# Kernel optimization log

Hardware: AMD Instinct MI355X
Metric: run time of the kernel (lower is better)

The kernel has to match this reference:

```python
import jax, jax.numpy as jnp
import numpy as np
import math

B, N, D, O, H = 8, 1024, 512, 512, 8
HD = O // H  # head_dim = 64


def setup_inputs() -> dict:
    key = jax.random.key(0)
    ks = jax.random.split(key, 12)
    x = jax.random.normal(ks[0], (B, N, D), dtype=jnp.float32)
    adj = jax.random.uniform(ks[1], (B, N, N), dtype=jnp.float32)  # unused by forward math
    mask = jax.random.randint(ks[2], (B, N), 0, 2) > 0  # bool padding mask
    # learned params (torch nn.Linear: y = x @ W.T + b)
    qkv_w = jax.random.normal(ks[3], (3 * O, D), dtype=jnp.float32) / math.sqrt(D)
    qkv_b = jnp.zeros((3 * O,), dtype=jnp.float32)
    # self_loop_W: 1/head_dim + U(0,1), per head, non-trainable
    self_loop_W = (1.0 / HD + jax.random.uniform(ks[4], (1, H, 1, 1))).astype(jnp.float32)
    w1 = jax.random.normal(ks[5], (O, O), dtype=jnp.float32) / math.sqrt(O)
    b1 = jnp.zeros((O,), dtype=jnp.float32)
    w2 = jax.random.normal(ks[6], (O, O), dtype=jnp.float32) / math.sqrt(O)
    b2 = jnp.zeros((O,), dtype=jnp.float32)
    wr = jax.random.normal(ks[7], (O, D), dtype=jnp.float32) / math.sqrt(D)
    br = jnp.zeros((O,), dtype=jnp.float32)
    return {"x": x, "adj": adj, "mask": mask, "self_loop_W": self_loop_W,
            "qkv_w": qkv_w, "qkv_b": qkv_b, "w1": w1, "b1": b1,
            "w2": w2, "b2": b2, "wr": wr, "br": br}


def reference(x, adj, mask, self_loop_W, qkv_w, qkv_b, w1, b1, w2, b2, wr, br):
    fmask = mask.astype(x.dtype)  # [B,N]
    # --- MoireAttention ---
    qkv = x @ qkv_w.T + qkv_b                       # [B,N,3O]
    qkv = qkv.reshape(B, N, 3, H, HD).transpose(2, 0, 3, 1, 4)  # [3,B,H,N,hd]
    Q, K, V = qkv[0], qkv[1], qkv[2]
    scores = jnp.einsum('bhnd,bhmd->bhnm', Q, K) / math.sqrt(HD)  # [B,H,N,N]
    eye = jnp.eye(N, dtype=scores.dtype)
    scores = scores + eye[None, None] * self_loop_W  # per-head diagonal self-loop bias
    mask2d = mask[:, None, :, None] & mask[:, None, None, :]  # [B,1,N,N]
    scores = jnp.where(mask2d, scores, jnp.asarray(-1e6, scores.dtype))
    attn = jax.nn.softmax(scores, axis=-1)
    h = jnp.einsum('bhnm,bhmd->bhnd', attn, V)      # [B,H,N,hd]
    h = h.transpose(0, 2, 1, 3).reshape(B, N, O)
    # --- mask, FFN (eval mode: noise/dropout are identity), mask ---
    h = h * fmask[..., None]
    h = jax.nn.relu(h @ w1.T + b1) @ w2.T + b2
    h = h * fmask[..., None]
    # --- residual blend ---
    x_proj = x @ wr.T + br
    return h * 0.5 + x_proj * 0.5
```

## Files before the change

### kernel.cpp

```cpp
#include <hip/hip_runtime.h>
#include <hip/hip_bf16.h>

typedef __attribute__((ext_vector_type(8))) short short8;
typedef __attribute__((ext_vector_type(4))) float f32x4;
typedef __attribute__((ext_vector_type(4))) short short4v;

#define BB 8
#define NN 1024
#define DD 512
#define OO 512
#define HH 8
#define HD 64
#define MM (BB * NN)

#define SEG_N 10
struct ConvArgs {
  const float* src[SEG_N];
  __hip_bfloat16* dst[SEG_N];
  int n4[SEG_N];
};

__global__ void convert_kernel(ConvArgs a) {
  const int t = blockIdx.y;
  const int n4 = a.n4[t];
  const float4* fs = (const float4*)a.src[t];
  short4v* d = (short4v*)a.dst[t];
  for (int i = blockIdx.x * blockDim.x + threadIdx.x; i < n4;
       i += gridDim.x * blockDim.x) {
    const float4 v = fs[i];
    union { short4v s; __hip_bfloat16 h[4]; } u;
    u.h[0] = __float2bfloat16(v.x);
    u.h[1] = __float2bfloat16(v.y);
    u.h[2] = __float2bfloat16(v.z);
    u.h[3] = __float2bfloat16(v.w);
    d[i] = u.s;
  }
}

template <int MODE>
__global__ __launch_bounds__(256) void gemm_bt(
    const __hip_bfloat16* __restrict__ A0, const __hip_bfloat16* __restrict__ B0,
    const __hip_bfloat16* __restrict__ A1, const __hip_bfloat16* __restrict__ B1,
    const __hip_bfloat16* __restrict__ bias0, const __hip_bfloat16* __restrict__ bias1,
    const int* __restrict__ mask,
    __hip_bfloat16* __restrict__ out0, __hip_bfloat16* __restrict__ out1,
    __hip_bfloat16* __restrict__ out2, float* __restrict__ outf,
    int M, int N, int Kd) {
  __shared__ __hip_bfloat16 As[128 * 40];
  __shared__ __hip_bfloat16 Bs[128 * 40];

  const int tid  = threadIdx.x;
  const int wave = tid >> 6;
  const int lane = tid & 63;
  const int fl   = lane & 15;
  const int fk   = (lane >> 4) * 8;
  const int wm   = (wave & 1) * 64;
  const int wn   = (wave >> 1) * 64;
  const int m0   = blockIdx.y * 128;
  const int n0   = blockIdx.x * 128;
  const int srow = tid >> 2;
  const int scol = (tid & 3) * 8;

  f32x4 acc[4][4];
#pragma unroll
  for (int i = 0; i < 4; ++i)
#pragma unroll
    for (int j = 0; j < 4; ++j) acc[i][j] = (f32x4){0.f, 0.f, 0.f, 0.f};

  const int npairs = (MODE == 2) ? 2 : 1;
  for (int p = 0; p < npairs; ++p) {
    const __hip_bfloat16* Ap = (p == 0) ? A0 : A1;
    const __hip_bfloat16* Bp = (p == 0) ? B0 : B1;
    for (int k0 = 0; k0 < Kd; k0 += 32) {
      __syncthreads();
      uint4 av0 = *(const uint4*)(Ap + (size_t)(m0 + srow) * Kd + k0 + scol);
      uint4 av1 = *(const uint4*)(Ap + (size_t)(m0 + srow + 64) * Kd + k0 + scol);
      uint4 bv0 = *(const uint4*)(Bp + (size_t)(n0 + srow) * Kd + k0 + scol);
      uint4 bv1 = *(const uint4*)(Bp + (size_t)(n0 + srow + 64) * Kd + k0 + scol);
      *(uint4*)&As[srow * 40 + scol] = av0;
      *(uint4*)&As[(srow + 64) * 40 + scol] = av1;
      *(uint4*)&Bs[srow * 40 + scol] = bv0;
      *(uint4*)&Bs[(srow + 64) * 40 + scol] = bv1;
      __syncthreads();

      short8 af[4], bfr[4];
#pragma unroll
      for (int i = 0; i < 4; ++i)
        af[i] = *(const short8*)&As[(wm + i * 16 + fl) * 40 + fk];
#pragma unroll
      for (int j = 0; j < 4; ++j)
        bfr[j] = *(const short8*)&Bs[(wn + j * 16 + fl) * 40 + fk];
#pragma unroll
      for (int i = 0; i < 4; ++i)
#pragma unroll
        for (int j = 0; j < 4; ++j)
          acc[i][j] = __builtin_amdgcn_mfma_f32_16x16x32_bf16(af[i], bfr[j],
                                                              acc[i][j], 0, 0, 0);
    }
  }

  const int rb = (lane >> 4) * 4;

  if (MODE == 0) {
#pragma unroll
    for (int j = 0; j < 4; ++j) {
      const int colb  = n0 + wn + j * 16;
      const int part  = colb >> 9;
      const int o     = colb & 511;
      const int headq = o >> 6;
      const int d     = (o & 63) + fl;
      const float bi  = __bfloat162float(bias0[colb + fl]);
      if (part < 2) {
        __hip_bfloat16* dst = (part == 0) ? out0 : out1;
#pragma unroll
        for (int i = 0; i < 4; ++i) {
#pragma unroll
          for (int r = 0; r < 4; ++r) {
            const int row = m0 + wm + i * 16 + rb + r;
            const int bb  = row >> 10;
            const int nn  = row & 1023;
            dst[((size_t)((bb << 3) + headq) * NN + nn) * HD + d] =
                __float2bfloat16(acc[i][j][r] + bi);
          }
        }
      } else {
#pragma unroll
        for (int i = 0; i < 4; ++i) {
#pragma unroll
          for (int r = 0; r < 4; ++r) {
            const int row = m0 + wm + i * 16 + rb + r;
            const int bb  = row >> 10;
            const int nn  = row & 1023;
            out2[((size_t)((bb << 3) + headq) * HD + d) * NN + nn] =
                __float2bfloat16(acc[i][j][r] + bi);
          }
        }
      }
    }
  } else if (MODE == 1) {
#pragma unroll
    for (int j = 0; j < 4; ++j) {
      const int col  = n0 + wn + j * 16 + fl;
      const float bi = __bfloat162float(bias0[col]);
#pragma unroll
      for (int i = 0; i < 4; ++i) {
#pragma unroll
        for (int r = 0; r < 4; ++r) {
          const int row = m0 + wm + i * 16 + rb + r;
          float v = fmaxf(acc[i][j][r] + bi, 0.f);
          if (mask[row] == 0) v = 0.f;
          out0[(size_t)row * N + col] = __float2bfloat16(v);
        }
      }
    }
  } else {
#pragma unroll
    for (int j = 0; j < 4; ++j) {
      const int col   = n0 + wn + j * 16 + fl;
      const float b2v = __bfloat162float(bias0[col]);
      const float brv = __bfloat162float(bias1[col]);
#pragma unroll
      for (int i = 0; i < 4; ++i) {
#pragma unroll
        for (int r = 0; r < 4; ++r) {
          const int row = m0 + wm + i * 16 + rb + r;
          const float v = acc[i][j][r] + brv + (mask[row] != 0 ? b2v : 0.f);
          outf[(size_t)row * N + col] = 0.5f * v;
        }
      }
    }
  }
}

__global__ __launch_bounds__(256) void attn_kernel(
    const __hip_bfloat16* __restrict__ Qb, const __hip_bfloat16* __restrict__ Kb,
    const __hip_bfloat16* __restrict__ Vt, const __hip_bfloat16* __restrict__ slw,
    const int* __restrict__ mask, __hip_bfloat16* __restrict__ hb) {
  __shared__ __hip_bfloat16 Qs[64 * 72];
  __shared__ __hip_bfloat16 Ks[64 * 72];
  __shared__ __hip_bfloat16 Vs[64 * 72];
  __shared__ __hip_bfloat16 Ps[64 * 72];
  __shared__ __hip_bfloat16 Ms[NN];

  const int tid  = threadIdx.x;
  const int wave = tid >> 6;
  const int lane = tid & 63;
  const int fl   = lane & 15;
  const int fk   = (lane >> 4) * 8;
  const int rb   = (lane >> 4) * 4;
  const int bh   = blockIdx.x >> 4;
  const int qblk = blockIdx.x & 15;
  const int b    = bh >> 3;
  const int head = bh & 7;
  const int q0   = qblk * 64;

  const float slw_h = __bfloat162float(slw[head]);

  const int srow = tid >> 2;
  const int sc   = (tid & 3) * 8;
  {
    const __hip_bfloat16* qg = Qb + ((size_t)bh * NN + q0) * HD;
    uint4 v0 = *(const uint4*)(qg + srow * HD + sc);
    uint4 v1 = *(const uint4*)(qg + srow * HD + sc + 32);
    *(uint4*)&Qs[srow * 72 + sc] = v0;
    *(uint4*)&Qs[srow * 72 + sc + 32] = v1;
#pragma unroll
    for (int k = 0; k < 4; ++k) {
      const int idx = tid * 4 + k;
      Ms[idx] = __float2bfloat16(mask[b * NN + idx] != 0 ? 1.f : 0.f);
    }
  }
  __syncthreads();
  const short8 qa0 = *(const short8*)&Qs[(wave * 16 + fl) * 72 + fk];
  const short8 qa1 = *(const short8*)&Qs[(wave * 16 + fl) * 72 + fk + 32];

  float lsum[4] = {0.f, 0.f, 0.f, 0.f};
  f32x4 Oacc[4];
#pragma unroll
  for (int t = 0; t < 4; ++t) Oacc[t] = (f32x4){0.f, 0.f, 0.f, 0.f};

  const float L2E = 1.44269504f;
  const float NEG = -11.54156032f;

  for (int kb = 0; kb < NN / 64; ++kb) {
    const int kbase = kb * 64;
    __syncthreads();
    {
      const __hip_bfloat16* kg = Kb + ((size_t)bh * NN + kbase) * HD;
      uint4 v0 = *(const uint4*)(kg + srow * HD + sc);
      uint4 v1 = *(const uint4*)(kg + srow * HD + sc + 32);
      *(uint4*)&Ks[srow * 72 + sc] = v0;
      *(uint4*)&Ks[srow * 72 + sc + 32] = v1;
      const __hip_bfloat16* vg = Vt + ((size_t)bh * HD + srow) * NN + kbase;
      uint4 w0 = *(const uint4*)(vg + sc);
      uint4 w1 = *(const uint4*)(vg + sc + 32);
      *(uint4*)&Vs[srow * 72 + sc] = w0;
      *(uint4*)&Vs[srow * 72 + sc + 32] = w1;
    }
    __syncthreads();

    f32x4 sfr[4];
#pragma unroll
    for (int j = 0; j < 4; ++j) {
      const short8 kf0 = *(const short8*)&Ks[(j * 16 + fl) * 72 + fk];
      const short8 kf1 = *(const short8*)&Ks[(j * 16 + fl) * 72 + fk + 32];
      f32x4 z = (f32x4){0.f, 0.f, 0.f, 0.f};
      z = __builtin_amdgcn_mfma_f32_16x16x32_bf16(qa0, kf0, z, 0, 0, 0);
      z = __builtin_amdgcn_mfma_f32_16x16x32_bf16(qa1, kf1, z, 0, 0, 0);
      sfr[j] = z;
    }

    float mv[4];
#pragma unroll
    for (int j = 0; j < 4; ++j)
      mv[j] = __bfloat162float(Ms[kbase + j * 16 + fl]);

#pragma unroll
    for (int r = 0; r < 4; ++r) {
      const int qrow_l = wave * 16 + rb + r;
      const int qrow_g = q0 + qrow_l;
#pragma unroll
      for (int j = 0; j < 4; ++j) {
        const int col_g = kbase + j * 16 + fl;
        float sv = sfr[j][r] * 0.125f;
        if (col_g == qrow_g) sv += slw_h;
        const float pv = mv[j] * exp2f(fmaf(sv, L2E, NEG));
        lsum[r] += pv;
        Ps[qrow_l * 72 + j * 16 + fl] = __float2bfloat16(pv);
      }
    }

    const short8 pa0 = *(const short8*)&Ps[(wave * 16 + fl) * 72 + fk];
    const short8 pa1 = *(const short8*)&Ps[(wave * 16 + fl) * 72 + fk + 32];
#pragma unroll
    for (int t = 0; t < 4; ++t) {
      const short8 vf0 = *(const short8*)&Vs[(t * 16 + fl) * 72 + fk];
      const short8 vf1 = *(const short8*)&Vs[(t * 16 + fl) * 72 + fk + 32];
      Oacc[t] = __builtin_amdgcn_mfma_f32_16x16x32_bf16(pa0, vf0, Oacc[t], 0, 0, 0);
      Oacc[t] = __builtin_amdgcn_mfma_f32_16x16x32_bf16(pa1, vf1, Oacc[t], 0, 0, 0);
    }
  }

  float scl[4];
#pragma unroll
  for (int r = 0; r < 4; ++r) {
    float l = lsum[r];
#pragma unroll
    for (int off = 1; off < 16; off <<= 1) l += __shfl_xor(l, off, 64);
    const int qrow_g = q0 + wave * 16 + rb + r;
    const float qm = (mask[b * NN + qrow_g] != 0) ? 1.f : 0.f;
    scl[r] = qm / fmaxf(l, 1e-30f);
  }
#pragma unroll
  for (int t = 0; t < 4; ++t) {
    const int d = t * 16 + fl;
#pragma unroll
    for (int r = 0; r < 4; ++r) {
      const int qrow_g = q0 + wave * 16 + rb + r;
      hb[(size_t)(b * NN + qrow_g) * OO + head * HD + d] =
          __float2bfloat16(Oacc[t][r] * scl[r]);
    }
  }
}

extern "C" void kernel_launch(void* const* d_in, const int* in_sizes, int n_in,
                              void* d_out, int out_size, void* d_ws, size_t ws_size,
                              hipStream_t stream) {
  const float* x_raw    = (const float*)d_in[0];
  const int* mask       = (const int*)d_in[2];
  const float* slw_raw  = (const float*)d_in[3];
  const float* qkvw_raw = (const float*)d_in[4];
  const float* qkvb_raw = (const float*)d_in[5];
  const float* w1_raw   = (const float*)d_in[6];
  const float* b1_raw   = (const float*)d_in[7];
  const float* w2_raw   = (const float*)d_in[8];
  const float* b2_raw   = (const float*)d_in[9];
  const float* wr_raw   = (const float*)d_in[10];
  const float* br_raw   = (const float*)d_in[11];
  float* outf           = (float*)d_out;

  __hip_bfloat16* p = (__hip_bfloat16*)d_ws;
  __hip_bfloat16* xc    = p; p += (size_t)MM * DD;
  __hip_bfloat16* qkvwc = p; p += 3 * OO * DD;
  __hip_bfloat16* w1c   = p; p += OO * OO;
  __hip_bfloat16* w2c   = p; p += OO * OO;
  __hip_bfloat16* wrc   = p; p += OO * DD;
  __hip_bfloat16* qkvbc = p; p += 3 * OO;
  __hip_bfloat16* b1c   = p; p += OO;
  __hip_bfloat16* b2c   = p; p += OO;
  __hip_bfloat16* brc   = p; p += OO;
  __hip_bfloat16* slwc  = p; p += 64;
  const size_t ebuf = (size_t)BB * HH * NN * HD;
  __hip_bfloat16* Qb = p; p += ebuf;
  __hip_bfloat16* Kb = p; p += ebuf;
  __hip_bfloat16* Vb = p; p += ebuf;
  __hip_bfloat16* hb = (__hip_bfloat16*)d_out;
  __hip_bfloat16* tb = Kb;

  if (ws_size < (size_t)((char*)p - (char*)d_ws)) return;

  ConvArgs ca;
  ca.src[0] = x_raw;    ca.dst[0] = xc;    ca.n4[0] = MM * DD / 4;
  ca.src[1] = qkvw_raw; ca.dst[1] = qkvwc; ca.n4[1] = 3 * OO * DD / 4;
  ca.src[2] = w1_raw;   ca.dst[2] = w1c;   ca.n4[2] = OO * OO / 4;
  ca.src[3] = w2_raw;   ca.dst[3] = w2c;   ca.n4[3] = OO * OO / 4;
  ca.src[4] = wr_raw;   ca.dst[4] = wrc;   ca.n4[4] = OO * DD / 4;
  ca.src[5] = qkvb_raw; ca.dst[5] = qkvbc; ca.n4[5] = 3 * OO / 4;
  ca.src[6] = b1_raw;   ca.dst[6] = b1c;   ca.n4[6] = OO / 4;
  ca.src[7] = b2_raw;   ca.dst[7] = b2c;   ca.n4[7] = OO / 4;
  ca.src[8] = br_raw;   ca.dst[8] = brc;   ca.n4[8] = OO / 4;
  ca.src[9] = slw_raw;  ca.dst[9] = slwc;  ca.n4[9] = HH / 4;
  convert_kernel<<<dim3(128, SEG_N), 256, 0, stream>>>(ca);

  gemm_bt<0><<<dim3(3 * OO / 128, MM / 128), 256, 0, stream>>>(
      xc, qkvwc, nullptr, nullptr, qkvbc, nullptr, mask, Qb, Kb, Vb, nullptr,
      MM, 3 * OO, DD);
  attn_kernel<<<BB * HH * (NN / 64), 256, 0, stream>>>(Qb, Kb, Vb, slwc, mask, hb);
  gemm_bt<1><<<dim3(OO / 128, MM / 128), 256, 0, stream>>>(
      hb, w1c, nullptr, nullptr, b1c, nullptr, mask, tb, nullptr, nullptr, nullptr,
      MM, OO, OO);
  gemm_bt<2><<<dim3(OO / 128, MM / 128), 256, 0, stream>>>(
      tb, w2c, xc, wrc, b2c, brc, mask, nullptr, nullptr, nullptr, outf,
      MM, OO, DD);
}
```

Baseline: 233.8 us.

## Fold softmax scale into Q, additive mask bias, and coalesced V-transpose stores

Pre-multiplies Q by 0.125*log2(e) in the QKV projection epilogue so the attention inner loop needs only an add and exp2, and replaces the multiplicative mask with an additive shift/large-negative bias stored as float in LDS. The diagonal self-loop check now runs only on the diagonal key block. The V-transposed output is staged through shared memory per wave so it can be written with 16-byte coalesced stores instead of scattered 2-byte writes. Risks: Q is rounded to bf16 after scaling, which perturbs precision slightly, and masked rows now get exp2(-30000)=0 rather than an exact zero multiply, which changes behaviour for fully masked rows.

```diff
diff --git a/kernel.cpp b/kernel.cpp
--- a/kernel.cpp
+++ b/kernel.cpp
@@ -12,6 +12,10 @@
 #define HH 8
 #define HD 64
 #define MM (BB * NN)
+
+#define QSC 0.18033688f
+#define KSHIFT -11.54156032f
+#define KMASKED -30000.0f
 
 #define SEG_N 10
 struct ConvArgs {
@@ -102,16 +106,17 @@
   const int rb = (lane >> 4) * 4;
 
   if (MODE == 0) {
-#pragma unroll
-    for (int j = 0; j < 4; ++j) {
-      const int colb  = n0 + wn + j * 16;
-      const int part  = colb >> 9;
-      const int o     = colb & 511;
-      const int headq = o >> 6;
-      const int d     = (o & 63) + fl;
-      const float bi  = __bfloat162float(bias0[colb + fl]);
-      if (part < 2) {
-        __hip_bfloat16* dst = (part == 0) ? out0 : out1;
+    const int part = n0 >> 9;
+    if (part < 2) {
+      __hip_bfloat16* dst = (part == 0) ? out0 : out1;
+      const float sc = (part == 0) ? QSC : 1.0f;
+#pragma unroll
+      for (int j = 0; j < 4; ++j) {
+        const int colb  = n0 + wn + j * 16;
+        const int o     = colb & 511;
+        const int headq = o >> 6;
+        const int d     = (o & 63) + fl;
+        const float bi  = __bfloat162float(bias0[colb + fl]);
 #pragma unroll
         for (int i = 0; i < 4; ++i) {
 #pragma unroll
@@ -120,21 +125,38 @@
             const int bb  = row >> 10;
             const int nn  = row & 1023;
             dst[((size_t)((bb << 3) + headq) * NN + nn) * HD + d] =
-                __float2bfloat16(acc[i][j][r] + bi);
+                __float2bfloat16((acc[i][j][r] + bi) * sc);
           }
         }
-      } else {
+      }
+    } else {
+      __syncthreads();
+      __hip_bfloat16* tsc = As + wave * 1120;
+      const int bb  = (m0 + wm) >> 10;
+      const int nnb = (m0 + wm) & 1023;
+      const int dl  = lane >> 2;
+      const int cc  = (lane & 3) * 16;
+#pragma unroll
+      for (int j = 0; j < 4; ++j) {
+        const int colb  = n0 + wn + j * 16;
+        const int o     = colb & 511;
+        const int headq = o >> 6;
+        const int dbase = o & 63;
+        const float bi  = __bfloat162float(bias0[colb + fl]);
 #pragma unroll
         for (int i = 0; i < 4; ++i) {
 #pragma unroll
           for (int r = 0; r < 4; ++r) {
-            const int row = m0 + wm + i * 16 + rb + r;
-            const int bb  = row >> 10;
-            const int nn  = row & 1023;
-            out2[((size_t)((bb << 3) + headq) * HD + d) * NN + nn] =
-                __float2bfloat16(acc[i][j][r] + bi);
+            const int rr = i * 16 + rb + r;
+            tsc[fl * 70 + rr] = __float2bfloat16(acc[i][j][r] + bi);
           }
         }
+        uint4 r0 = *(const uint4*)&tsc[dl * 70 + cc];
+        uint4 r1 = *(const uint4*)&tsc[dl * 70 + cc + 8];
+        __hip_bfloat16* vdst =
+            out2 + ((size_t)((bb << 3) + headq) * HD + dbase + dl) * NN + nnb;
+        *(uint4*)&vdst[cc] = r0;
+        *(uint4*)&vdst[cc + 8] = r1;
       }
     }
   } else if (MODE == 1) {
@@ -180,7 +202,7 @@
   __shared__ __hip_bfloat16 Ks[64 * 72];
   __shared__ __hip_bfloat16 Vs[64 * 72];
   __shared__ __hip_bfloat16 Ps[64 * 72];
-  __shared__ __hip_bfloat16 Ms[NN];
+  __shared__ float Msf[NN];
 
   const int tid  = threadIdx.x;
   const int wave = tid >> 6;
@@ -194,7 +216,7 @@
   const int head = bh & 7;
   const int q0   = qblk * 64;
 
-  const float slw_h = __bfloat162float(slw[head]);
+  const float slwL2 = __bfloat162float(slw[head]) * 1.44269504f;
 
   const int srow = tid >> 2;
   const int sc   = (tid & 3) * 8;
@@ -207,7 +229,7 @@
 #pragma unroll
     for (int k = 0; k < 4; ++k) {
       const int idx = tid * 4 + k;
-      Ms[idx] = __float2bfloat16(mask[b * NN + idx] != 0 ? 1.f : 0.f);
+      Msf[idx] = (mask[b * NN + idx] != 0) ? KSHIFT : KMASKED;
     }
   }
   __syncthreads();
@@ -218,9 +240,6 @@
   f32x4 Oacc[4];
 #pragma unroll
   for (int t = 0; t < 4; ++t) Oacc[t] = (f32x4){0.f, 0.f, 0.f, 0.f};
-
-  const float L2E = 1.44269504f;
-  const float NEG = -11.54156032f;
 
   for (int kb = 0; kb < NN / 64; ++kb) {
     const int kbase = kb * 64;
@@ -250,23 +269,33 @@
       sfr[j] = z;
     }
 
-    float mv[4];
-#pragma unroll
-    for (int j = 0; j < 4; ++j)
-      mv[j] = __bfloat162float(Ms[kbase + j * 16 + fl]);
-
-#pragma unroll
-    for (int r = 0; r < 4; ++r) {
-      const int qrow_l = wave * 16 + rb + r;
-      const int qrow_g = q0 + qrow_l;
-#pragma unroll
-      for (int j = 0; j < 4; ++j) {
-        const int col_g = kbase + j * 16 + fl;
-        float sv = sfr[j][r] * 0.125f;
-        if (col_g == qrow_g) sv += slw_h;
-        const float pv = mv[j] * exp2f(fmaf(sv, L2E, NEG));
-        lsum[r] += pv;
-        Ps[qrow_l * 72 + j * 16 + fl] = __float2bfloat16(pv);
+    float mb[4];
+#pragma unroll
+    for (int j = 0; j < 4; ++j) mb[j] = Msf[kbase + j * 16 + fl];
+
+    if (kb != qblk) {
+#pragma unroll
+      for (int r = 0; r < 4; ++r) {
+        const int qrow_l = wave * 16 + rb + r;
+#pragma unroll
+        for (int j = 0; j < 4; ++j) {
+          const float pv = exp2f(sfr[j][r] + mb[j]);
+          lsum[r] += pv;
+          Ps[qrow_l * 72 + j * 16 + fl] = __float2bfloat16(pv);
+        }
+      }
+    } else {
+#pragma unroll
+      for (int r = 0; r < 4; ++r) {
+        const int qrow_l = wave * 16 + rb + r;
+#pragma unroll
+        for (int j = 0; j < 4; ++j) {
+          float sv = sfr[j][r] + mb[j];
+          if (j * 16 + fl == qrow_l) sv += slwL2;
+          const float pv = exp2f(sv);
+          lsum[r] += pv;
+          Ps[qrow_l * 72 + j * 16 + fl] = __float2bfloat16(pv);
+        }
       }
     }
 
```

Result: no change. 231.0 us (-1.2%).
